# Kernel optimization log

Hardware: AMD Instinct MI355X
Metric: run time of the kernel (lower is better)

Reference implementation:

```python
import jax, jax.numpy as jnp
import numpy as np

N = 50000       # population nodes
E = 1_600_000   # edges per edge type
F_IN = 2000     # flattened individual-graph embedding (100*20)
D = 20          # hidden channels per TransformerConv head (heads=1)
NEG_SLOPE = 0.01
BN_EPS = 1e-5


def setup_inputs() -> dict:
    key = jax.random.key(0)
    ks = jax.random.split(key, 24)
    features = jax.random.normal(ks[0], (N, F_IN), jnp.float32)
    same_index = jax.random.randint(ks[1], (2, E), 0, N, dtype=jnp.int64)
    diff_index = jax.random.randint(ks[2], (2, E), 0, N, dtype=jnp.int64)
    s0 = 1.0 / np.sqrt(F_IN)
    s1 = 1.0 / np.sqrt(D)
    # layer 0 conv params, stacked over the 2 edge types (same, diff)
    W0q = jax.random.normal(ks[3], (2, F_IN, D), jnp.float32) * s0
    W0k = jax.random.normal(ks[4], (2, F_IN, D), jnp.float32) * s0
    W0v = jax.random.normal(ks[5], (2, F_IN, D), jnp.float32) * s0
    W0s = jax.random.normal(ks[6], (2, F_IN, D), jnp.float32) * s0
    b0q = jnp.zeros((2, D)); b0k = jnp.zeros((2, D))
    b0v = jnp.zeros((2, D)); b0s = jnp.zeros((2, D))
    # layers 1..3 conv params: [layer, edge_type, D, D]
    Wq = jax.random.normal(ks[7], (3, 2, D, D), jnp.float32) * s1
    Wk = jax.random.normal(ks[8], (3, 2, D, D), jnp.float32) * s1
    Wv = jax.random.normal(ks[9], (3, 2, D, D), jnp.float32) * s1
    Ws = jax.random.normal(ks[10], (3, 2, D, D), jnp.float32) * s1
    bq = jnp.zeros((3, 2, D)); bk = jnp.zeros((3, 2, D))
    bv = jnp.zeros((3, 2, D)); bs = jnp.zeros((3, 2, D))
    w1 = jnp.full((4,), 0.8, jnp.float32)
    w2 = jnp.full((4,), 0.2, jnp.float32)
    bn_gamma = jnp.ones((4, D), jnp.float32)
    bn_beta = jnp.zeros((4, D), jnp.float32)
    Wout = jax.random.normal(ks[11], (4 * D, 2), jnp.float32) / np.sqrt(4 * D)
    bout = jnp.zeros((2,), jnp.float32)
    return dict(features=features, same_index=same_index, diff_index=diff_index,
                W0q=W0q, b0q=b0q, W0k=W0k, b0k=b0k, W0v=W0v, b0v=b0v, W0s=W0s, b0s=b0s,
                Wq=Wq, bq=bq, Wk=Wk, bk=bk, Wv=Wv, bv=bv, Ws=Ws, bs=bs,
                w1=w1, w2=w2, bn_gamma=bn_gamma, bn_beta=bn_beta, Wout=Wout, bout=bout)


def _tconv(x, edge_index, Wq, bq, Wk, bk, Wv, bv, Ws, bs):
    """PyG TransformerConv, heads=1, concat=True, root_weight=True, no edge_attr."""
    src, dst = edge_index[0], edge_index[1]
    q = x @ Wq + bq   # [N, D]
    k = x @ Wk + bk
    v = x @ Wv + bv
    logits = jnp.einsum('ed,ed->e', q[dst], k[src]) / jnp.sqrt(jnp.float32(D))  # [E]
    m = jax.ops.segment_max(logits, dst, num_segments=N)
    m = jnp.where(jnp.isfinite(m), m, jnp.float32(0.0))  # nodes with no in-edges
    e = jnp.exp(logits - m[dst])
    z = jax.ops.segment_sum(e, dst, num_segments=N)
    alpha = e / (z[dst] + 1e-16)  # PyG softmax epsilon
    agg = jax.ops.segment_sum(alpha[:, None] * v[src], dst, num_segments=N)  # [N, D]
    return agg + x @ Ws + bs  # skip (root) connection


def _bn(x, gamma, beta):
    mu = x.mean(axis=0)
    var = x.var(axis=0)
    return (x - mu) * jax.lax.rsqrt(var + BN_EPS) * gamma + beta


def reference(features, same_index, diff_index,
              W0q, b0q, W0k, b0k, W0v, b0v, W0s, b0s,
              Wq, bq, Wk, bk, Wv, bv, Ws, bs,
              w1, w2, bn_gamma, bn_beta, Wout, bout):
    x = features
    fcs = []
    for l in range(4):
        if l == 0:
            p_same = (W0q[0], b0q[0], W0k[0], b0k[0], W0v[0], b0v[0], W0s[0], b0s[0])
            p_diff = (W0q[1], b0q[1], W0k[1], b0k[1], W0v[1], b0v[1], W0s[1], b0s[1])
        else:
            i = l - 1
            p_same = (Wq[i, 0], bq[i, 0], Wk[i, 0], bk[i, 0], Wv[i, 0], bv[i, 0], Ws[i, 0], bs[i, 0])
            p_diff = (Wq[i, 1], bq[i, 1], Wk[i, 1], bk[i, 1], Wv[i, 1], bv[i, 1], Ws[i, 1], bs[i, 1])
        x1 = _tconv(x, same_index, *p_same)
        x2 = _tconv(x, diff_index, *p_diff)
        t = w1[l] + w2[l]
        x = (w1[l] / t) * x1 + (w2[l] / t) * x2
        x = _bn(x, bn_gamma[l], bn_beta[l])
        x = jax.nn.leaky_relu(x, NEG_SLOPE)
        fcs.append(x)
    fc = jnp.concatenate(fcs, axis=-1)  # [N, 80]
    return fc @ Wout + bout  # [N, 2]
```

## Files before the change

### kernel.cpp

```cpp
#include <hip/hip_runtime.h>
#include <math.h>

#define N_NODES 50000
#define E_EDGES 1600000
#define F_IN    2000
#define D       20
#define NCOL    160
#define KPAD    2016
#define NBNP    64

#define INV_SQRT_D 0.22360679774997896f

typedef __bf16 bf16x8 __attribute__((ext_vector_type(8)));
typedef __bf16 bf16x4 __attribute__((ext_vector_type(4)));
typedef float  f32x4  __attribute__((ext_vector_type(4)));

__global__ void pack_kernel(
    const float* __restrict__ W0q, const float* __restrict__ W0k,
    const float* __restrict__ W0v, const float* __restrict__ W0s,
    const float* __restrict__ b0q, const float* __restrict__ b0k,
    const float* __restrict__ b0v, const float* __restrict__ b0s,
    const float* __restrict__ Wq,  const float* __restrict__ Wk,
    const float* __restrict__ Wv,  const float* __restrict__ Ws_,
    const float* __restrict__ bq,  const float* __restrict__ bk,
    const float* __restrict__ bv,  const float* __restrict__ bs_,
    __bf16* __restrict__ B0, float* __restrict__ bias0,
    float* __restrict__ WL, float* __restrict__ biasL,
    float* __restrict__ bnp, int* __restrict__ deg)
{
  long idx = (long)blockIdx.x * blockDim.x + threadIdx.x;
  if (idx < (long)NCOL*KPAD) {
    int col = (int)(idx / KPAD), k = (int)(idx % KPAD);
    int et = col / 80, r = col % 80, mat = r / 20, d = r % 20;
    const float* w = (mat==0)?W0q:(mat==1)?W0s:(mat==2)?W0k:W0v;
    float v = (k < F_IN) ? w[((size_t)et*F_IN + k)*D + d] : 0.f;
    B0[idx] = (__bf16)v;
    return;
  }
  idx -= (long)NCOL*KPAD;
  if (idx < 160) {
    int col = (int)idx;
    int et = col / 80, r = col % 80, mat = r / 20, d = r % 20;
    const float* b = (mat==0)?b0q:(mat==1)?b0s:(mat==2)?b0k:b0v;
    bias0[col] = b[et*D + d];
    return;
  }
  idx -= 160;
  if (idx < 9600) {
    int l = (int)(idx / 3200), rem = (int)(idx % 3200);
    int k = rem / NCOL, col = rem % NCOL;
    int et = col / 80, r = col % 80, mat = r / 20, d = r % 20;
    const float* w = (mat==0)?Wq:(mat==1)?Ws_:(mat==2)?Wk:Wv;
    WL[idx] = w[(((size_t)l*2 + et)*D + k)*D + d];
    return;
  }
  idx -= 9600;
  if (idx < 480) {
    int l = (int)(idx / NCOL), col = (int)(idx % NCOL);
    int et = col / 80, r = col % 80, mat = r / 20, d = r % 20;
    const float* b = (mat==0)?bq:(mat==1)?bs_:(mat==2)?bk:bv;
    biasL[idx] = b[(l*2 + et)*D + d];
    return;
  }
  idx -= 480;
  if (idx < 4*NBNP*40) { bnp[idx] = 0.f; return; }
  idx -= 4*NBNP*40;
  if (idx < 2*N_NODES) { deg[idx] = 0; return; }
}

__global__ void hist_kernel(const int* __restrict__ same, const int* __restrict__ diff,
                            int* __restrict__ deg)
{
  long i = (long)blockIdx.x * blockDim.x + threadIdx.x;
  if (i >= 2L*E_EDGES) return;
  int et = (i >= E_EDGES) ? 1 : 0;
  long e = i - (long)et*E_EDGES;
  const int* ix = et ? diff : same;
  int dst = ix[E_EDGES + e];
  atomicAdd(&deg[(size_t)et*N_NODES + dst], 1);
}

__global__ void scan_kernel(const int* __restrict__ deg,
                            int* __restrict__ rowptr0, int* __restrict__ rowptr1,
                            int* __restrict__ next0, int* __restrict__ next1)
{
  const int et = blockIdx.x;
  const int* dg = deg + (size_t)et*N_NODES;
  int* rp = et ? rowptr1 : rowptr0;
  int* np = et ? next1 : next0;
  __shared__ int part[1024];
  const int t = threadIdx.x;
  const int per = (N_NODES + 1023) / 1024;
  const int b = t * per;
  const int e = (b + per < N_NODES) ? (b + per) : N_NODES;
  int s = 0;
  for (int i = b; i < e; i++) s += dg[i];
  part[t] = s;
  __syncthreads();
  for (int o = 1; o < 1024; o <<= 1) {
    int v = (t >= o) ? part[t-o] : 0;
    __syncthreads();
    part[t] += v;
    __syncthreads();
  }
  int run = (t == 0) ? 0 : part[t-1];
  for (int i = b; i < e; i++) {
    rp[i] = run; np[i] = run;
    run += dg[i];
  }
  if (t == 0) rp[N_NODES] = part[1023];
}

#define SC_EPT 16
#define SC_CHUNK (256*SC_EPT)
__global__ void scatter_kernel(const int* __restrict__ same, const int* __restrict__ diff,
                               int* __restrict__ next0, int* __restrict__ next1,
                               int* __restrict__ adj0, int* __restrict__ adj1)
{
  const int part  = blockIdx.x & 7;
  const int chunk = blockIdx.x >> 3;
  const int lo = part * (N_NODES/8);
  const int hi = lo + (N_NODES/8);
  const long i0 = (long)chunk * SC_CHUNK + threadIdx.x;
#pragma unroll
  for (int it = 0; it < SC_EPT; ++it) {
    long i = i0 + (long)it*256;
    if (i >= 2L*E_EDGES) break;
    int et = (i >= E_EDGES) ? 1 : 0;
    long e = i - (long)et*E_EDGES;
    const int* ix = et ? diff : same;
    int dst = ix[E_EDGES + e];
    if (dst >= lo && dst < hi) {
      int src = ix[e];
      int* np  = et ? next1 : next0;
      int* adj = et ? adj1  : adj0;
      int pos = atomicAdd(&np[dst], 1);
      adj[pos] = src;
    }
  }
}

__launch_bounds__(512)
__global__ void gemm0_mfma(const float* __restrict__ A,
                           const __bf16* __restrict__ Bt,
                           const float* __restrict__ bias,
                           __bf16* __restrict__ C)
{
  __shared__ __bf16 as[128*32];
  const int t    = threadIdx.x;
  const int lane = t & 63;
  const int wid  = t >> 6;
  const int wr   = wid >> 1;
  const int wc   = wid & 1;
  const int rb0  = blockIdx.x * 128;

  const int srow = t >> 2;
  const int skc  = (t & 3) * 8;
  const int arow = rb0 + srow;
  const float* aptr = A + (size_t)arow * F_IN;

  const int lrow = lane & 15;
  const int lkb  = (lane >> 4) * 8;

  f32x4 acc[2][5];
#pragma unroll
  for (int i = 0; i < 2; i++)
#pragma unroll
    for (int j = 0; j < 5; j++) acc[i][j] = (f32x4){0.f,0.f,0.f,0.f};

  float4 p0, p1;
  auto loadA = [&](int k0) {
    int k = k0 + skc;
    if (arow < N_NODES) {
      if (k + 8 <= F_IN) {
        p0 = *(const float4*)(aptr + k);
        p1 = *(const float4*)(aptr + k + 4);
      } else {
        float tmp[8];
#pragma unroll
        for (int i = 0; i < 8; i++) tmp[i] = (k + i < F_IN) ? aptr[k + i] : 0.f;
        p0 = make_float4(tmp[0],tmp[1],tmp[2],tmp[3]);
        p1 = make_float4(tmp[4],tmp[5],tmp[6],tmp[7]);
      }
    } else {
      p0 = make_float4(0,0,0,0); p1 = p0;
    }
  };

  loadA(0);
  for (int s = 0; s < 63; s++) {
    bf16x8 h;
    h[0]=(__bf16)p0.x; h[1]=(__bf16)p0.y; h[2]=(__bf16)p0.z; h[3]=(__bf16)p0.w;
    h[4]=(__bf16)p1.x; h[5]=(__bf16)p1.y; h[6]=(__bf16)p1.z; h[7]=(__bf16)p1.w;
    *(bf16x8*)&as[srow*32 + skc] = h;
    __syncthreads();
    if (s + 1 < 63) loadA((s + 1) * 32);

    bf16x8 af[2];
#pragma unroll
    for (int rf = 0; rf < 2; rf++)
      af[rf] = *(bf16x8*)&as[(wr*32 + rf*16 + lrow)*32 + lkb];
    bf16x8 bfr[5];
#pragma unroll
    for (int cf = 0; cf < 5; cf++)
      bfr[cf] = *(const bf16x8*)(Bt + (size_t)(wc*80 + cf*16 + lrow)*KPAD + s*32 + lkb);
#pragma unroll
    for (int rf = 0; rf < 2; rf++)
#pragma unroll
      for (int cf = 0; cf < 5; cf++)
        acc[rf][cf] = __builtin_amdgcn_mfma_f32_16x16x32_bf16(af[rf], bfr[cf], acc[rf][cf], 0, 0, 0);
    __syncthreads();
  }

#pragma unroll
  for (int rf = 0; rf < 2; rf++) {
#pragma unroll
    for (int cf = 0; cf < 5; cf++) {
      int col = wc*80 + cf*16 + lrow;
      float bv = bias[col];
#pragma unroll
      for (int j = 0; j < 4; j++) {
        int r = rb0 + wr*32 + rf*16 + (lane >> 4)*4 + j;
        if (r < N_NODES) C[(size_t)r*NCOL + col] = (__bf16)(acc[rf][cf][j] + bv);
      }
    }
  }
}

__launch_bounds__(256)
__global__ void proj_small_kernel(const float* __restrict__ xp, const float* __restrict__ bnl,
                                  const float* __restrict__ gam, const float* __restrict__ bet,
                                  const float* __restrict__ W, const float* __restrict__ bias,
                                  __bf16* __restrict__ C)
{
  __shared__ float ws[20*160];
  __shared__ float xs[16*20];
  __shared__ float Ac[20], Bc[20];
  const int t = threadIdx.x;
  const int n0 = blockIdx.x * 16;
#pragma unroll
  for (int i = 0; i < 13; i++) {
    int idx = t + i*256;
    if (idx < 3200) ws[idx] = W[idx];
  }
  if (t < 20) {
    float s1 = 0.f, s2 = 0.f;
    for (int s = 0; s < NBNP; s++) { s1 += bnl[s*40 + t]; s2 += bnl[s*40 + 20 + t]; }
    float mu  = s1 * (1.f/N_NODES);
    float var = s2 * (1.f/N_NODES) - mu*mu;
    float a = rsqrtf(var + 1e-5f) * gam[t];
    Ac[t] = a; Bc[t] = bet[t] - mu*a;
  }
  __syncthreads();
#pragma unroll
  for (int i = 0; i < 2; i++) {
    int idx = t + i*256;
    if (idx < 320) {
      int nl = idx / 20, k = idx % 20;
      int n = n0 + nl;
      float x = (n < N_NODES) ? xp[(size_t)n*D + k] : 0.f;
      float y = x*Ac[k] + Bc[k];
      xs[idx] = (y > 0.f) ? y : 0.01f*y;
    }
  }
  __syncthreads();
#pragma unroll
  for (int i = 0; i < 10; i++) {
    int idx = t + i*256;
    int nl = idx / NCOL, col = idx % NCOL;
    int n = n0 + nl;
    if (n < N_NODES) {
      float acc = bias[col];
#pragma unroll
      for (int k = 0; k < 20; k++) acc += xs[nl*20 + k] * ws[k*NCOL + col];
      C[(size_t)n*NCOL + col] = (__bf16)acc;
    }
  }
}

__launch_bounds__(256)
__global__ void attn_fused(const int* __restrict__ rp0, const int* __restrict__ adj0,
                           const int* __restrict__ rp1, const int* __restrict__ adj1,
                           const __bf16* __restrict__ proj,
                           const float* __restrict__ w1, const float* __restrict__ w2, int l,
                           float* __restrict__ xpre, float* __restrict__ bnp)
{
  __shared__ float xnode[4][20];
  const int t    = threadIdx.x;
  const int wv   = t >> 6;
  const int lane = t & 63;
  const int half = lane >> 5;
  const int sl   = lane & 31;
  const int node = blockIdx.x*4 + wv;

  const int* rowptr = half ? rp1 : rp0;
  const int* adj    = half ? adj1 : adj0;
  const __bf16* rq  = proj + (size_t)node*NCOL + half*80;

  float qf[20];
  {
    bf16x8 q0 = *(const bf16x8*)(rq);
    bf16x8 q1 = *(const bf16x8*)(rq + 8);
    bf16x4 q2 = *(const bf16x4*)(rq + 16);
#pragma unroll
    for (int i = 0; i < 8; i++) { qf[i] = (float)q0[i]; qf[8+i] = (float)q1[i]; }
#pragma unroll
    for (int i = 0; i < 4; i++) qf[16+i] = (float)q2[i];
  }

  const int beg = rowptr[node], end = rowptr[node+1];
  float z = 0.f;
  float S[20];
#pragma unroll
  for (int d = 0; d < 20; d++) S[d] = 0.f;

  for (int i = beg + sl; i < end; i += 32) {
    const int src = adj[i];
    const __bf16* kv = proj + (size_t)src*NCOL + half*80 + 40;
    bf16x8 a0 = *(const bf16x8*)(kv);
    bf16x8 a1 = *(const bf16x8*)(kv + 8);
    bf16x8 a2 = *(const bf16x8*)(kv + 16);
    bf16x8 a3 = *(const bf16x8*)(kv + 24);
    bf16x8 a4 = *(const bf16x8*)(kv + 32);
    float d0 = 0.f;
#pragma unroll
    for (int j = 0; j < 8; j++) d0 += qf[j]     * (float)a0[j];
#pragma unroll
    for (int j = 0; j < 8; j++) d0 += qf[8 + j] * (float)a1[j];
#pragma unroll
    for (int j = 0; j < 4; j++) d0 += qf[16 + j]* (float)a2[j];
    const float w0 = __expf(fminf(d0*INV_SQRT_D, 80.f));
    z += w0;
#pragma unroll
    for (int d = 0; d < 4; d++) S[d]     += w0*(float)a2[4+d];
#pragma unroll
    for (int d = 0; d < 8; d++) S[4+d]   += w0*(float)a3[d];
#pragma unroll
    for (int d = 0; d < 8; d++) S[12+d]  += w0*(float)a4[d];
  }

#pragma unroll
  for (int o = 16; o >= 1; o >>= 1) {
    z += __shfl_xor(z, o, 64);
#pragma unroll
    for (int d = 0; d < 20; d++) S[d] += __shfl_xor(S[d], o, 64);
  }

  const float inv = (z > 0.f) ? 1.f/z : 0.f;
  float outv[20];
  {
    bf16x4 s0 = *(const bf16x4*)(rq + 20);
    bf16x8 s1 = *(const bf16x8*)(rq + 24);
    bf16x8 s2 = *(const bf16x8*)(rq + 32);
#pragma unroll
    for (int i = 0; i < 4; i++) outv[i] = S[i]*inv + (float)s0[i];
#pragma unroll
    for (int i = 0; i < 8; i++) { outv[4+i]  = S[4+i]*inv  + (float)s1[i];
                                  outv[12+i] = S[12+i]*inv + (float)s2[i]; }
  }

  const float wa = w1[l], wb = w2[l];
  const float c0 = wa/(wa+wb), c1 = wb/(wa+wb);
  const float cme = half ? c1 : c0;
  const float cot = half ? c0 : c1;
  float x[20];
#pragma unroll
  for (int d = 0; d < 20; d++) {
    float o2 = __shfl_xor(outv[d], 32, 64);
    x[d] = cme*outv[d] + cot*o2;
  }

  if (lane == 0) {
    float* xo = xpre + (size_t)node*D;
#pragma unroll
    for (int j = 0; j < 5; j++) {
      float4 o4 = make_float4(x[4*j], x[4*j+1], x[4*j+2], x[4*j+3]);
      *(float4*)(xo + 4*j) = o4;
    }
#pragma unroll
    for (int d = 0; d < 20; d++) xnode[wv][d] = x[d];
  }
  __syncthreads();

  if (t < 20) {
    float s1 = xnode[0][t] + xnode[1][t] + xnode[2][t] + xnode[3][t];
    float s2 = xnode[0][t]*xnode[0][t] + xnode[1][t]*xnode[1][t]
             + xnode[2][t]*xnode[2][t] + xnode[3][t]*xnode[3][t];
    float* slot = bnp + (blockIdx.x & (NBNP-1))*40;
    atomicAdd(&slot[t], s1);
    atomicAdd(&slot[20 + t], s2);
  }
}

__launch_bounds__(256)
__global__ void final_kernel(const float* __restrict__ xpre4, const float* __restrict__ bnp,
                             const float* __restrict__ gam, const float* __restrict__ bet,
                             const float* __restrict__ Wout, const float* __restrict__ bout,
                             float* __restrict__ out)
{
  __shared__ float Ac[80], Bc[80], wlds[160];
  const int t = threadIdx.x;
  if (t < 80) {
    int l = t / 20, d = t % 20;
    const float* b = bnp + l*(NBNP*40);
    float s1 = 0.f, s2 = 0.f;
    for (int s = 0; s < NBNP; s++) { s1 += b[s*40 + d]; s2 += b[s*40 + 20 + d]; }
    float mu  = s1 * (1.f/N_NODES);
    float var = s2 * (1.f/N_NODES) - mu*mu;
    float a = rsqrtf(var + 1e-5f) * gam[t];
    Ac[t] = a; Bc[t] = bet[t] - mu*a;
  }
  if (t < 160) wlds[t] = Wout[t];
  __syncthreads();

  const int n = blockIdx.x*256 + t;
  if (n >= N_NODES) return;
  float a0 = bout[0], a1 = bout[1];
#pragma unroll
  for (int l = 0; l < 4; l++) {
    const float* base = xpre4 + (size_t)l*N_NODES*D + (size_t)n*D;
#pragma unroll
    for (int d = 0; d < D; d++) {
      int idx = l*20 + d;
      float y = base[d]*Ac[idx] + Bc[idx];
      y = (y > 0.f) ? y : 0.01f*y;
      a0 += y * wlds[idx*2 + 0];
      a1 += y * wlds[idx*2 + 1];
    }
  }
  out[n*2+0] = a0;
  out[n*2+1] = a1;
}

extern "C" void kernel_launch(void* const* d_in, const int* in_sizes, int n_in,
                              void* d_out, int out_size, void* d_ws, size_t ws_size,
                              hipStream_t stream)
{
  const float* feat = (const float*)d_in[0];
  const int*   same = (const int*)d_in[1];
  const int*   diff = (const int*)d_in[2];
  const float* W0q = (const float*)d_in[3];
  const float* b0q = (const float*)d_in[4];
  const float* W0k = (const float*)d_in[5];
  const float* b0k = (const float*)d_in[6];
  const float* W0v = (const float*)d_in[7];
  const float* b0v = (const float*)d_in[8];
  const float* W0s = (const float*)d_in[9];
  const float* b0s = (const float*)d_in[10];
  const float* Wq  = (const float*)d_in[11];
  const float* bq  = (const float*)d_in[12];
  const float* Wk  = (const float*)d_in[13];
  const float* bk  = (const float*)d_in[14];
  const float* Wv  = (const float*)d_in[15];
  const float* bv  = (const float*)d_in[16];
  const float* Ws_ = (const float*)d_in[17];
  const float* bs_ = (const float*)d_in[18];
  const float* w1  = (const float*)d_in[19];
  const float* w2  = (const float*)d_in[20];
  const float* gamma = (const float*)d_in[21];
  const float* beta  = (const float*)d_in[22];
  const float* Wout  = (const float*)d_in[23];
  const float* bout  = (const float*)d_in[24];

  float* wsf  = (float*)d_ws;
  __bf16*  PROJ  = (__bf16*)wsf;
  float*   XPRE4 = wsf + 4000000;
  __bf16*  B0bf  = (__bf16*)(wsf + 8000000);
  float*   BIAS0 = wsf + 8161280;
  float*   WL    = wsf + 8161440;
  float*   BIASL = wsf + 8171040;
  float*   BNP   = wsf + 8171520;
  int*     ib    = (int*)(wsf + 8181760);
  int* DEG  = ib;
  int* RP0  = ib + 100000;
  int* RP1  = ib + 150004;
  int* NX0  = ib + 200008;
  int* NX1  = ib + 250008;
  int* ADJ0 = ib + 300008;
  int* ADJ1 = ib + 1900008;

  const int packN = NCOL*KPAD + 160 + 9600 + 480 + 4*NBNP*40 + 2*N_NODES;
  pack_kernel<<<(packN + 255)/256, 256, 0, stream>>>(
      W0q, W0k, W0v, W0s, b0q, b0k, b0v, b0s,
      Wq, Wk, Wv, Ws_, bq, bk, bv, bs_,
      B0bf, BIAS0, WL, BIASL, BNP, DEG);

  hist_kernel<<<(2*E_EDGES + 255)/256, 256, 0, stream>>>(same, diff, DEG);
  scan_kernel<<<2, 1024, 0, stream>>>(DEG, RP0, RP1, NX0, NX1);
  {
    const long nchunk = (2L*E_EDGES + SC_CHUNK - 1) / SC_CHUNK;
    scatter_kernel<<<(int)(nchunk*8), 256, 0, stream>>>(same, diff, NX0, NX1, ADJ0, ADJ1);
  }

  for (int l = 0; l < 4; l++) {
    if (l == 0)
      gemm0_mfma<<<(N_NODES + 127)/128, 512, 0, stream>>>(feat, B0bf, BIAS0, PROJ);
    else
      proj_small_kernel<<<(N_NODES + 15)/16, 256, 0, stream>>>(
          XPRE4 + (size_t)(l-1)*N_NODES*D, BNP + (l-1)*(NBNP*40),
          gamma + (l-1)*D, beta + (l-1)*D,
          WL + (size_t)(l-1)*3200, BIASL + (size_t)(l-1)*160, PROJ);

    attn_fused<<<N_NODES/4, 256, 0, stream>>>(
        RP0, ADJ0, RP1, ADJ1, PROJ, w1, w2, l,
        XPRE4 + (size_t)l*N_NODES*D, BNP + l*(NBNP*40));
  }

  final_kernel<<<(N_NODES + 255)/256, 256, 0, stream>>>(
      XPRE4, BNP, gamma, beta, Wout, bout, (float*)d_out);
}
```

Measured before the change: 988.9 us.

## Split projection buffer into separate Q/skip and per-edge-type 128B-aligned KV arrays

The single per-node projection buffer (160 bf16 per row) is split into a Q/skip array and two key/value arrays, one per edge type, each padded to 64 bf16 (128 bytes) per row. The attention gather then reads each source node's K/V from one compact, aligned row instead of a 40-element slice at an offset within a 320-byte row. The goal is fewer cache lines and less wasted bandwidth per random gather. In exchange the GEMM and projection epilogues write scattered, non-contiguous stores with extra index arithmetic, and the workspace layout grows.

```diff
diff --git a/kernel.cpp b/kernel.cpp
--- a/kernel.cpp
+++ b/kernel.cpp
@@ -14,6 +14,7 @@
 typedef __bf16 bf16x8 __attribute__((ext_vector_type(8)));
 typedef __bf16 bf16x4 __attribute__((ext_vector_type(4)));
 typedef float  f32x4  __attribute__((ext_vector_type(4)));
+
 
 __global__ void pack_kernel(
     const float* __restrict__ W0q, const float* __restrict__ W0k,
@@ -144,7 +145,8 @@
 __global__ void gemm0_mfma(const float* __restrict__ A,
                            const __bf16* __restrict__ Bt,
                            const float* __restrict__ bias,
-                           __bf16* __restrict__ C)
+                           __bf16* __restrict__ QS,
+                           __bf16* __restrict__ KV0, __bf16* __restrict__ KV1)
 {
   __shared__ __bf16 as[128*32];
   const int t    = threadIdx.x;
@@ -217,11 +219,17 @@
 #pragma unroll
     for (int cf = 0; cf < 5; cf++) {
       int col = wc*80 + cf*16 + lrow;
+      int et = col / 80, r = col % 80, mat = r / 20, d = r % 20;
       float bv = bias[col];
+      __bf16* kvp = et ? KV1 : KV0;
 #pragma unroll
       for (int j = 0; j < 4; j++) {
-        int r = rb0 + wr*32 + rf*16 + (lane >> 4)*4 + j;
-        if (r < N_NODES) C[(size_t)r*NCOL + col] = (__bf16)(acc[rf][cf][j] + bv);
+        int row = rb0 + wr*32 + rf*16 + (lane >> 4)*4 + j;
+        if (row < N_NODES) {
+          __bf16 val = (__bf16)(acc[rf][cf][j] + bv);
+          if (mat < 2) QS[(size_t)row*80 + et*40 + mat*20 + d] = val;
+          else         kvp[(size_t)row*64 + (mat-2)*20 + d]   = val;
+        }
       }
     }
   }
@@ -231,7 +239,8 @@
 __global__ void proj_small_kernel(const float* __restrict__ xp, const float* __restrict__ bnl,
                                   const float* __restrict__ gam, const float* __restrict__ bet,
                                   const float* __restrict__ W, const float* __restrict__ bias,
-                                  __bf16* __restrict__ C)
+                                  __bf16* __restrict__ QS,
+                                  __bf16* __restrict__ KV0, __bf16* __restrict__ KV1)
 {
   __shared__ float ws[20*160];
   __shared__ float xs[16*20];
@@ -273,7 +282,10 @@
       float acc = bias[col];
 #pragma unroll
       for (int k = 0; k < 20; k++) acc += xs[nl*20 + k] * ws[k*NCOL + col];
-      C[(size_t)n*NCOL + col] = (__bf16)acc;
+      int et = col / 80, r = col % 80, mat = r / 20, d = r % 20;
+      __bf16 val = (__bf16)acc;
+      if (mat < 2) QS[(size_t)n*80 + et*40 + mat*20 + d] = val;
+      else         (et ? KV1 : KV0)[(size_t)n*64 + (mat-2)*20 + d] = val;
     }
   }
 }
@@ -281,7 +293,8 @@
 __launch_bounds__(256)
 __global__ void attn_fused(const int* __restrict__ rp0, const int* __restrict__ adj0,
                            const int* __restrict__ rp1, const int* __restrict__ adj1,
-                           const __bf16* __restrict__ proj,
+                           const __bf16* __restrict__ QS,
+                           const __bf16* __restrict__ KV0, const __bf16* __restrict__ KV1,
                            const float* __restrict__ w1, const float* __restrict__ w2, int l,
                            float* __restrict__ xpre, float* __restrict__ bnp)
 {
@@ -295,7 +308,8 @@
 
   const int* rowptr = half ? rp1 : rp0;
   const int* adj    = half ? adj1 : adj0;
-  const __bf16* rq  = proj + (size_t)node*NCOL + half*80;
+  const __bf16* kvb = half ? KV1 : KV0;
+  const __bf16* rq  = QS + (size_t)node*80 + half*40;
 
   float qf[20];
   {
@@ -316,7 +330,7 @@
 
   for (int i = beg + sl; i < end; i += 32) {
     const int src = adj[i];
-    const __bf16* kv = proj + (size_t)src*NCOL + half*80 + 40;
+    const __bf16* kv = kvb + (size_t)src*64;
     bf16x8 a0 = *(const bf16x8*)(kv);
     bf16x8 a1 = *(const bf16x8*)(kv + 8);
     bf16x8 a2 = *(const bf16x8*)(kv + 16);
@@ -463,14 +477,16 @@
   const float* bout  = (const float*)d_in[24];
 
   float* wsf  = (float*)d_ws;
-  __bf16*  PROJ  = (__bf16*)wsf;
-  float*   XPRE4 = wsf + 4000000;
-  __bf16*  B0bf  = (__bf16*)(wsf + 8000000);
-  float*   BIAS0 = wsf + 8161280;
-  float*   WL    = wsf + 8161440;
-  float*   BIASL = wsf + 8171040;
-  float*   BNP   = wsf + 8171520;
-  int*     ib    = (int*)(wsf + 8181760);
+  __bf16*  QS    = (__bf16*)wsf;
+  __bf16*  KV0   = (__bf16*)(wsf + 2000000);
+  __bf16*  KV1   = (__bf16*)(wsf + 3600000);
+  float*   XPRE4 = wsf + 5200000;
+  __bf16*  B0bf  = (__bf16*)(wsf + 9200000);
+  float*   BIAS0 = wsf + 9361280;
+  float*   WL    = wsf + 9361440;
+  float*   BIASL = wsf + 9371040;
+  float*   BNP   = wsf + 9371520;
+  int*     ib    = (int*)(wsf + 9381760);
   int* DEG  = ib;
   int* RP0  = ib + 100000;
   int* RP1  = ib + 150004;
@@ -494,15 +510,15 @@
 
   for (int l = 0; l < 4; l++) {
     if (l == 0)
-      gemm0_mfma<<<(N_NODES + 127)/128, 512, 0, stream>>>(feat, B0bf, BIAS0, PROJ);
+      gemm0_mfma<<<(N_NODES + 127)/128, 512, 0, stream>>>(feat, B0bf, BIAS0, QS, KV0, KV1);
     else
       proj_small_kernel<<<(N_NODES + 15)/16, 256, 0, stream>>>(
           XPRE4 + (size_t)(l-1)*N_NODES*D, BNP + (l-1)*(NBNP*40),
           gamma + (l-1)*D, beta + (l-1)*D,
-          WL + (size_t)(l-1)*3200, BIASL + (size_t)(l-1)*160, PROJ);
+          WL + (size_t)(l-1)*3200, BIASL + (size_t)(l-1)*160, QS, KV0, KV1);
 
     attn_fused<<<N_NODES/4, 256, 0, stream>>>(
-        RP0, ADJ0, RP1, ADJ1, PROJ, w1, w2, l,
+        RP0, ADJ0, RP1, ADJ1, QS, KV0, KV1, w1, w2, l,
         XPRE4 + (size_t)l*N_NODES*D, BNP + l*(NBNP*40));
   }
 
```

Measured after the change: 986.9 us. Within noise of the previous version (-0.2%).

## Split projections into 128-byte Q/S and K/V records, restructure attention gather

Applied to the files above, without the earlier changes.

Projections are now written into two padded layouts: per-node Q|S records and per-edge-type K|V records of 64 bf16 each, so every neighbour gather reads one aligned 128-byte row. The attention kernel now has 8-lane teams handle one edge each, with a shuffle reduction for the dot product, instead of one lane per edge holding 20-wide vectors. The histogram kernel uses the same destination-partitioned chunking as the scatter kernel to localise atomics, and the layer-0 GEMM uses 64-row tiles with 256 threads. The padded layout uses more memory and needs extra zero-initialisation, and the BN statistics now use per-node atomics rather than per-block ones, which raises the atomic count.

```diff
diff --git a/kernel.cpp b/kernel.cpp
--- a/kernel.cpp
+++ b/kernel.cpp
@@ -12,8 +12,8 @@
 #define INV_SQRT_D 0.22360679774997896f
 
 typedef __bf16 bf16x8 __attribute__((ext_vector_type(8)));
-typedef __bf16 bf16x4 __attribute__((ext_vector_type(4)));
 typedef float  f32x4  __attribute__((ext_vector_type(4)));
+
 
 __global__ void pack_kernel(
     const float* __restrict__ W0q, const float* __restrict__ W0k,
@@ -26,7 +26,8 @@
     const float* __restrict__ bv,  const float* __restrict__ bs_,
     __bf16* __restrict__ B0, float* __restrict__ bias0,
     float* __restrict__ WL, float* __restrict__ biasL,
-    float* __restrict__ bnp, int* __restrict__ deg)
+    float* __restrict__ bnp, int* __restrict__ deg,
+    __bf16* __restrict__ KV)
 {
   long idx = (long)blockIdx.x * blockDim.x + threadIdx.x;
   if (idx < (long)NCOL*KPAD) {
@@ -66,18 +67,32 @@
   if (idx < 4*NBNP*40) { bnp[idx] = 0.f; return; }
   idx -= 4*NBNP*40;
   if (idx < 2*N_NODES) { deg[idx] = 0; return; }
-}
+  idx -= 2*N_NODES;
+  if (idx < 2L*N_NODES*64) { KV[idx] = (__bf16)0.f; return; }
+}
+
+#define SC_EPT 16
+#define SC_CHUNK (256*SC_EPT)
 
 __global__ void hist_kernel(const int* __restrict__ same, const int* __restrict__ diff,
                             int* __restrict__ deg)
 {
-  long i = (long)blockIdx.x * blockDim.x + threadIdx.x;
-  if (i >= 2L*E_EDGES) return;
-  int et = (i >= E_EDGES) ? 1 : 0;
-  long e = i - (long)et*E_EDGES;
-  const int* ix = et ? diff : same;
-  int dst = ix[E_EDGES + e];
-  atomicAdd(&deg[(size_t)et*N_NODES + dst], 1);
+  const int part  = blockIdx.x & 7;
+  const int chunk = blockIdx.x >> 3;
+  const int lo = part * (N_NODES/8);
+  const int hi = lo + (N_NODES/8);
+  const long i0 = (long)chunk * SC_CHUNK + threadIdx.x;
+#pragma unroll
+  for (int it = 0; it < SC_EPT; ++it) {
+    long i = i0 + (long)it*256;
+    if (i >= 2L*E_EDGES) break;
+    int et = (i >= E_EDGES) ? 1 : 0;
+    long e = i - (long)et*E_EDGES;
+    const int* ix = et ? diff : same;
+    int dst = ix[E_EDGES + e];
+    if (dst >= lo && dst < hi)
+      atomicAdd(&deg[(size_t)et*N_NODES + dst], 1);
+  }
 }
 
 __global__ void scan_kernel(const int* __restrict__ deg,
@@ -111,8 +126,6 @@
   if (t == 0) rp[N_NODES] = part[1023];
 }
 
-#define SC_EPT 16
-#define SC_CHUNK (256*SC_EPT)
 __global__ void scatter_kernel(const int* __restrict__ same, const int* __restrict__ diff,
                                int* __restrict__ next0, int* __restrict__ next1,
                                int* __restrict__ adj0, int* __restrict__ adj1)
@@ -140,19 +153,19 @@
   }
 }
 
-__launch_bounds__(512)
+__launch_bounds__(256)
 __global__ void gemm0_mfma(const float* __restrict__ A,
                            const __bf16* __restrict__ Bt,
                            const float* __restrict__ bias,
-                           __bf16* __restrict__ C)
-{
-  __shared__ __bf16 as[128*32];
+                           __bf16* __restrict__ QS2, __bf16* __restrict__ KV)
+{
+  __shared__ __bf16 as[64*32];
   const int t    = threadIdx.x;
   const int lane = t & 63;
   const int wid  = t >> 6;
   const int wr   = wid >> 1;
   const int wc   = wid & 1;
-  const int rb0  = blockIdx.x * 128;
+  const int rb0  = blockIdx.x * 64;
 
   const int srow = t >> 2;
   const int skc  = (t & 3) * 8;
@@ -217,11 +230,16 @@
 #pragma unroll
     for (int cf = 0; cf < 5; cf++) {
       int col = wc*80 + cf*16 + lrow;
+      int et = col / 80, r = col % 80, mat = r / 20, d = r % 20;
       float bv = bias[col];
 #pragma unroll
       for (int j = 0; j < 4; j++) {
-        int r = rb0 + wr*32 + rf*16 + (lane >> 4)*4 + j;
-        if (r < N_NODES) C[(size_t)r*NCOL + col] = (__bf16)(acc[rf][cf][j] + bv);
+        int row = rb0 + wr*32 + rf*16 + (lane >> 4)*4 + j;
+        if (row < N_NODES) {
+          __bf16 val = (__bf16)(acc[rf][cf][j] + bv);
+          if (mat < 2) QS2[((size_t)row*2 + et)*64 + (mat==1 ? 32 : 0) + d] = val;
+          else         KV[((size_t)et*N_NODES + row)*64 + (mat==3 ? 32 : 0) + d] = val;
+        }
       }
     }
   }
@@ -231,7 +249,7 @@
 __global__ void proj_small_kernel(const float* __restrict__ xp, const float* __restrict__ bnl,
                                   const float* __restrict__ gam, const float* __restrict__ bet,
                                   const float* __restrict__ W, const float* __restrict__ bias,
-                                  __bf16* __restrict__ C)
+                                  __bf16* __restrict__ QS2, __bf16* __restrict__ KV)
 {
   __shared__ float ws[20*160];
   __shared__ float xs[16*20];
@@ -273,7 +291,10 @@
       float acc = bias[col];
 #pragma unroll
       for (int k = 0; k < 20; k++) acc += xs[nl*20 + k] * ws[k*NCOL + col];
-      C[(size_t)n*NCOL + col] = (__bf16)acc;
+      int et = col / 80, r = col % 80, mat = r / 20, d = r % 20;
+      __bf16 val = (__bf16)acc;
+      if (mat < 2) QS2[((size_t)n*2 + et)*64 + (mat==1 ? 32 : 0) + d] = val;
+      else         KV[((size_t)et*N_NODES + n)*64 + (mat==3 ? 32 : 0) + d] = val;
     }
   }
 }
@@ -281,114 +302,108 @@
 __launch_bounds__(256)
 __global__ void attn_fused(const int* __restrict__ rp0, const int* __restrict__ adj0,
                            const int* __restrict__ rp1, const int* __restrict__ adj1,
-                           const __bf16* __restrict__ proj,
+                           const __bf16* __restrict__ QS2, const __bf16* __restrict__ KV,
                            const float* __restrict__ w1, const float* __restrict__ w2, int l,
                            float* __restrict__ xpre, float* __restrict__ bnp)
 {
-  __shared__ float xnode[4][20];
   const int t    = threadIdx.x;
   const int wv   = t >> 6;
   const int lane = t & 63;
-  const int half = lane >> 5;
-  const int sl   = lane & 31;
+  const int team = lane >> 3;
+  const int j    = lane & 7;
   const int node = blockIdx.x*4 + wv;
 
-  const int* rowptr = half ? rp1 : rp0;
-  const int* adj    = half ? adj1 : adj0;
-  const __bf16* rq  = proj + (size_t)node*NCOL + half*80;
-
-  float qf[20];
-  {
-    bf16x8 q0 = *(const bf16x8*)(rq);
-    bf16x8 q1 = *(const bf16x8*)(rq + 8);
-    bf16x4 q2 = *(const bf16x4*)(rq + 16);
-#pragma unroll
-    for (int i = 0; i < 8; i++) { qf[i] = (float)q0[i]; qf[8+i] = (float)q1[i]; }
-#pragma unroll
-    for (int i = 0; i < 4; i++) qf[16+i] = (float)q2[i];
-  }
-
-  const int beg = rowptr[node], end = rowptr[node+1];
-  float z = 0.f;
-  float S[20];
-#pragma unroll
-  for (int d = 0; d < 20; d++) S[d] = 0.f;
-
-  for (int i = beg + sl; i < end; i += 32) {
-    const int src = adj[i];
-    const __bf16* kv = proj + (size_t)src*NCOL + half*80 + 40;
-    bf16x8 a0 = *(const bf16x8*)(kv);
-    bf16x8 a1 = *(const bf16x8*)(kv + 8);
-    bf16x8 a2 = *(const bf16x8*)(kv + 16);
-    bf16x8 a3 = *(const bf16x8*)(kv + 24);
-    bf16x8 a4 = *(const bf16x8*)(kv + 32);
-    float d0 = 0.f;
-#pragma unroll
-    for (int j = 0; j < 8; j++) d0 += qf[j]     * (float)a0[j];
-#pragma unroll
-    for (int j = 0; j < 8; j++) d0 += qf[8 + j] * (float)a1[j];
-#pragma unroll
-    for (int j = 0; j < 4; j++) d0 += qf[16 + j]* (float)a2[j];
-    const float w0 = __expf(fminf(d0*INV_SQRT_D, 80.f));
-    z += w0;
-#pragma unroll
-    for (int d = 0; d < 4; d++) S[d]     += w0*(float)a2[4+d];
-#pragma unroll
-    for (int d = 0; d < 8; d++) S[4+d]   += w0*(float)a3[d];
-#pragma unroll
-    for (int d = 0; d < 8; d++) S[12+d]  += w0*(float)a4[d];
-  }
-
-#pragma unroll
-  for (int o = 16; o >= 1; o >>= 1) {
-    z += __shfl_xor(z, o, 64);
-#pragma unroll
-    for (int d = 0; d < 20; d++) S[d] += __shfl_xor(S[d], o, 64);
-  }
-
-  const float inv = (z > 0.f) ? 1.f/z : 0.f;
-  float outv[20];
-  {
-    bf16x4 s0 = *(const bf16x4*)(rq + 20);
-    bf16x8 s1 = *(const bf16x8*)(rq + 24);
-    bf16x8 s2 = *(const bf16x8*)(rq + 32);
-#pragma unroll
-    for (int i = 0; i < 4; i++) outv[i] = S[i]*inv + (float)s0[i];
-#pragma unroll
-    for (int i = 0; i < 8; i++) { outv[4+i]  = S[4+i]*inv  + (float)s1[i];
-                                  outv[12+i] = S[12+i]*inv + (float)s2[i]; }
+  float out[2][8];
+
+#pragma unroll
+  for (int et = 0; et < 2; ++et) {
+    const int* rowptr = et ? rp1 : rp0;
+    const int* adj    = et ? adj1 : adj0;
+    const __bf16* kvb = KV + (size_t)et*N_NODES*64;
+
+    float qd[8], sv[8];
+    {
+      bf16x8 qsv = *(const bf16x8*)(QS2 + ((size_t)node*2 + et)*64 + 8*j);
+#pragma unroll
+      for (int i = 0; i < 8; i++) {
+        float f = (float)qsv[i];
+        qd[i] = (j < 4) ? f : 0.f;
+        sv[i] = f;
+      }
+    }
+
+    const int beg = rowptr[node], endi = rowptr[node+1];
+    float z = 0.f, Sp[8];
+#pragma unroll
+    for (int i = 0; i < 8; i++) Sp[i] = 0.f;
+
+    for (int base = beg; base < endi; base += 64) {
+      const int adjv = adj[base + lane];
+      const int ne = endi - base;
+      const int nloc = (ne < 64) ? ne : 64;
+      for (int r = 0; r*8 < nloc; ++r) {
+        const int eidx = r*8 + team;
+        const bool val = eidx < nloc;
+        const int src = __shfl(adjv, eidx, 64);
+        bf16x8 kvv = *(const bf16x8*)(kvb + (size_t)(val ? src : 0)*64 + 8*j);
+        float kf[8];
+#pragma unroll
+        for (int i = 0; i < 8; i++) kf[i] = (float)kvv[i];
+        float pd = 0.f;
+#pragma unroll
+        for (int i = 0; i < 8; i++) pd += qd[i]*kf[i];
+        pd += __shfl_xor(pd, 1, 64);
+        pd += __shfl_xor(pd, 2, 64);
+        pd += __shfl_xor(pd, 4, 64);
+        float w = __expf(fminf(pd*INV_SQRT_D, 80.f));
+        w = val ? w : 0.f;
+        z += w;
+#pragma unroll
+        for (int i = 0; i < 8; i++) Sp[i] += w*kf[i];
+      }
+    }
+
+#pragma unroll
+    for (int o = 8; o <= 32; o <<= 1) {
+      z += __shfl_xor(z, o, 64);
+#pragma unroll
+      for (int i = 0; i < 8; i++) Sp[i] += __shfl_xor(Sp[i], o, 64);
+    }
+
+    const float inv = (z > 0.f) ? 1.f/z : 0.f;
+#pragma unroll
+    for (int i = 0; i < 8; i++) out[et][i] = Sp[i]*inv + sv[i];
   }
 
   const float wa = w1[l], wb = w2[l];
   const float c0 = wa/(wa+wb), c1 = wb/(wa+wb);
-  const float cme = half ? c1 : c0;
-  const float cot = half ? c0 : c1;
-  float x[20];
-#pragma unroll
-  for (int d = 0; d < 20; d++) {
-    float o2 = __shfl_xor(outv[d], 32, 64);
-    x[d] = cme*outv[d] + cot*o2;
-  }
-
-  if (lane == 0) {
+  float x[8];
+#pragma unroll
+  for (int i = 0; i < 8; i++) x[i] = c0*out[0][i] + c1*out[1][i];
+
+  if (team == 0) {
     float* xo = xpre + (size_t)node*D;
-#pragma unroll
-    for (int j = 0; j < 5; j++) {
-      float4 o4 = make_float4(x[4*j], x[4*j+1], x[4*j+2], x[4*j+3]);
-      *(float4*)(xo + 4*j) = o4;
-    }
-#pragma unroll
-    for (int d = 0; d < 20; d++) xnode[wv][d] = x[d];
-  }
-  __syncthreads();
-
-  if (t < 20) {
-    float s1 = xnode[0][t] + xnode[1][t] + xnode[2][t] + xnode[3][t];
-    float s2 = xnode[0][t]*xnode[0][t] + xnode[1][t]*xnode[1][t]
-             + xnode[2][t]*xnode[2][t] + xnode[3][t]*xnode[3][t];
-    float* slot = bnp + (blockIdx.x & (NBNP-1))*40;
-    atomicAdd(&slot[t], s1);
-    atomicAdd(&slot[20 + t], s2);
+    if (j == 4) {
+      *(float4*)(xo)     = make_float4(x[0],x[1],x[2],x[3]);
+      *(float4*)(xo + 4) = make_float4(x[4],x[5],x[6],x[7]);
+    } else if (j == 5) {
+      *(float4*)(xo + 8)  = make_float4(x[0],x[1],x[2],x[3]);
+      *(float4*)(xo + 12) = make_float4(x[4],x[5],x[6],x[7]);
+    } else if (j == 6) {
+      *(float4*)(xo + 16) = make_float4(x[0],x[1],x[2],x[3]);
+    }
+    if (j >= 4 && j <= 6) {
+      float* slot = bnp + (size_t)(node & (NBNP-1))*40;
+      const int dbase = (j-4)*8;
+      const int cnt = (j==6) ? 4 : 8;
+#pragma unroll
+      for (int i = 0; i < 8; i++) {
+        if (i < cnt) {
+          atomicAdd(&slot[dbase + i], x[i]);
+          atomicAdd(&slot[20 + dbase + i], x[i]*x[i]);
+        }
+      }
+    }
   }
 }
 
@@ -463,14 +478,15 @@
   const float* bout  = (const float*)d_in[24];
 
   float* wsf  = (float*)d_ws;
-  __bf16*  PROJ  = (__bf16*)wsf;
-  float*   XPRE4 = wsf + 4000000;
-  __bf16*  B0bf  = (__bf16*)(wsf + 8000000);
-  float*   BIAS0 = wsf + 8161280;
-  float*   WL    = wsf + 8161440;
-  float*   BIASL = wsf + 8171040;
-  float*   BNP   = wsf + 8171520;
-  int*     ib    = (int*)(wsf + 8181760);
+  __bf16*  QS2   = (__bf16*)wsf;
+  __bf16*  KV    = (__bf16*)(wsf + 3200000);
+  float*   XPRE4 = wsf + 6400000;
+  __bf16*  B0bf  = (__bf16*)(wsf + 10400000);
+  float*   BIAS0 = wsf + 10561280;
+  float*   WL    = wsf + 10561440;
+  float*   BIASL = wsf + 10571040;
+  float*   BNP   = wsf + 10571520;
+  int*     ib    = (int*)(wsf + 10581760);
   int* DEG  = ib;
   int* RP0  = ib + 100000;
   int* RP1  = ib + 150004;
@@ -479,30 +495,29 @@
   int* ADJ0 = ib + 300008;
   int* ADJ1 = ib + 1900008;
 
-  const int packN = NCOL*KPAD + 160 + 9600 + 480 + 4*NBNP*40 + 2*N_NODES;
-  pack_kernel<<<(packN + 255)/256, 256, 0, stream>>>(
+  const long packN = (long)NCOL*KPAD + 160 + 9600 + 480 + 4*NBNP*40 + 2*N_NODES
+                   + 2L*N_NODES*64;
+  pack_kernel<<<(int)((packN + 255)/256), 256, 0, stream>>>(
       W0q, W0k, W0v, W0s, b0q, b0k, b0v, b0s,
       Wq, Wk, Wv, Ws_, bq, bk, bv, bs_,
-      B0bf, BIAS0, WL, BIASL, BNP, DEG);
-
-  hist_kernel<<<(2*E_EDGES + 255)/256, 256, 0, stream>>>(same, diff, DEG);
+      B0bf, BIAS0, WL, BIASL, BNP, DEG, KV);
+
+  const long nchunk = (2L*E_EDGES + SC_CHUNK - 1) / SC_CHUNK;
+  hist_kernel<<<(int)(nchunk*8), 256, 0, stream>>>(same, diff, DEG);
   scan_kernel<<<2, 1024, 0, stream>>>(DEG, RP0, RP1, NX0, NX1);
-  {
-    const long nchunk = (2L*E_EDGES + SC_CHUNK - 1) / SC_CHUNK;
-    scatter_kernel<<<(int)(nchunk*8), 256, 0, stream>>>(same, diff, NX0, NX1, ADJ0, ADJ1);
-  }
+  scatter_kernel<<<(int)(nchunk*8), 256, 0, stream>>>(same, diff, NX0, NX1, ADJ0, ADJ1);
 
   for (int l = 0; l < 4; l++) {
     if (l == 0)
-      gemm0_mfma<<<(N_NODES + 127)/128, 512, 0, stream>>>(feat, B0bf, BIAS0, PROJ);
+      gemm0_mfma<<<(N_NODES + 63)/64, 256, 0, stream>>>(feat, B0bf, BIAS0, QS2, KV);
     else
       proj_small_kernel<<<(N_NODES + 15)/16, 256, 0, stream>>>(
           XPRE4 + (size_t)(l-1)*N_NODES*D, BNP + (l-1)*(NBNP*40),
           gamma + (l-1)*D, beta + (l-1)*D,
-          WL + (size_t)(l-1)*3200, BIASL + (size_t)(l-1)*160, PROJ);
+          WL + (size_t)(l-1)*3200, BIASL + (size_t)(l-1)*160, QS2, KV);
 
     attn_fused<<<N_NODES/4, 256, 0, stream>>>(
-        RP0, ADJ0, RP1, ADJ1, PROJ, w1, w2, l,
+        RP0, ADJ0, RP1, ADJ1, QS2, KV, w1, w2, l,
         XPRE4 + (size_t)l*N_NODES*D, BNP + l*(NBNP*40));
   }
 
```

New measurement: 1.852 ms. +87.3%, slower.
